# Performance work log

Hardware: AMD Instinct MI355X
Metric: run time of the kernel (lower is better)

The kernel has to match this reference:

```python
import jax, jax.numpy as jnp
import numpy as np

B, L, D = 16, 2048, 64

def setup_inputs() -> dict:
    key = jax.random.key(0)
    kq, kk, kv = jax.random.split(key, 3)
    q = jax.random.normal(kq, (B, L, D), dtype=jnp.float32)
    k = jax.random.normal(kk, (B, L, D), dtype=jnp.float32)
    v = jax.random.normal(kv, (B, L, D), dtype=jnp.float32)
    return {"q": q, "k": k, "v": v}

def reference(q, k, v):
    # scores: [B, L_q, L_k] = q @ k^T  (no scale applied, faithful to source)
    scores = jnp.einsum("bqd,bkd->bqk", q, k)
    attention = jax.nn.softmax(scores, axis=2)
    # dropout p=0.0 -> identity
    # source returns (v, attention), NOT the context
    return (v, attention)
```

## Files before the change

kernel.cpp:

```cpp
#include <hip/hip_runtime.h>
#include <hip/hip_bf16.h>

typedef short s16x8 __attribute__((ext_vector_type(8)));
typedef float f32x4 __attribute__((ext_vector_type(4)));

#define B_ 16
#define L_ 2048
#define D_ 64
#define V_ELEMS (B_ * L_ * D_)

__device__ __forceinline__ unsigned rne1(float f) {
    unsigned u = __builtin_bit_cast(unsigned, f);
    return (u + 0x7FFFu + ((u >> 16) & 1u)) >> 16;
}
__device__ __forceinline__ unsigned pack2(float a, float b) {
    return (rne1(a) & 0xFFFFu) | (rne1(b) << 16);
}

__device__ __forceinline__ void split8(float4 a, float4 b, s16x8& hi, s16x8& lo) {
    float f[8] = {a.x, a.y, a.z, a.w, b.x, b.y, b.z, b.w};
    s16x8 h, l;
#pragma unroll
    for (int i = 0; i < 8; ++i) {
        unsigned u = __builtin_bit_cast(unsigned, f[i]);
        h[i] = (short)(u >> 16);
        float lf = f[i] - __builtin_bit_cast(float, u & 0xFFFF0000u);
        l[i] = (short)rne1(lf);
    }
    hi = h; lo = l;
}

__global__ void copy_v_kernel(const float4* __restrict__ v, float4* __restrict__ o) {
    int i = blockIdx.x * blockDim.x + threadIdx.x;
    o[i] = v[i];
}

__global__ void prep_qk_kernel(const float4* __restrict__ q, const float4* __restrict__ k,
                               uint2* __restrict__ qhi, uint2* __restrict__ qlo,
                               uint2* __restrict__ khi, uint2* __restrict__ klo) {
    int i = blockIdx.x * blockDim.x + threadIdx.x;
    float4 fq = q[i];
    float4 fk = k[i];
    unsigned u0 = __builtin_bit_cast(unsigned, fq.x), u1 = __builtin_bit_cast(unsigned, fq.y);
    unsigned u2 = __builtin_bit_cast(unsigned, fq.z), u3 = __builtin_bit_cast(unsigned, fq.w);
    qhi[i] = make_uint2((u0 >> 16) | (u1 & 0xFFFF0000u), (u2 >> 16) | (u3 & 0xFFFF0000u));
    qlo[i] = make_uint2(
        pack2(fq.x - __builtin_bit_cast(float, u0 & 0xFFFF0000u),
              fq.y - __builtin_bit_cast(float, u1 & 0xFFFF0000u)),
        pack2(fq.z - __builtin_bit_cast(float, u2 & 0xFFFF0000u),
              fq.w - __builtin_bit_cast(float, u3 & 0xFFFF0000u)));
    u0 = __builtin_bit_cast(unsigned, fk.x); u1 = __builtin_bit_cast(unsigned, fk.y);
    u2 = __builtin_bit_cast(unsigned, fk.z); u3 = __builtin_bit_cast(unsigned, fk.w);
    khi[i] = make_uint2((u0 >> 16) | (u1 & 0xFFFF0000u), (u2 >> 16) | (u3 & 0xFFFF0000u));
    klo[i] = make_uint2(
        pack2(fk.x - __builtin_bit_cast(float, u0 & 0xFFFF0000u),
              fk.y - __builtin_bit_cast(float, u1 & 0xFFFF0000u)),
        pack2(fk.z - __builtin_bit_cast(float, u2 & 0xFFFF0000u),
              fk.w - __builtin_bit_cast(float, u3 & 0xFFFF0000u)));
}

__device__ __forceinline__ void store4f(float* p, unsigned u0, unsigned u1, float inv) {
    float4 w;
    w.x = __builtin_bit_cast(float, u0 << 16) * inv;
    w.y = __builtin_bit_cast(float, u0 & 0xFFFF0000u) * inv;
    w.z = __builtin_bit_cast(float, u1 << 16) * inv;
    w.w = __builtin_bit_cast(float, u1 & 0xFFFF0000u) * inv;
    *(float4*)p = w;
}

template <bool PRE>
__global__ __launch_bounds__(256, 2) void attn_kernel(
    const float* __restrict__ qf, const float* __restrict__ kf,
    const ushort* __restrict__ qhi, const ushort* __restrict__ qlo,
    const ushort* __restrict__ khi, const ushort* __restrict__ klo,
    float* __restrict__ og) {
    const int b    = blockIdx.x >> 6;
    const int q0   = (blockIdx.x & 63) << 5;
    const int tid  = threadIdx.x;
    const int wave = tid >> 6;
    const int lane = tid & 63;
    const int nq   = lane & 15;
    const int quad = lane >> 4;

    s16x8 bhi[2][2], blo[2][2];
#pragma unroll
    for (int t = 0; t < 2; ++t) {
        const size_t off = ((size_t)(b * L_ + q0 + t * 16 + nq)) * D_ + quad * 8;
        if constexpr (PRE) {
            bhi[t][0] = *(const s16x8*)(qhi + off);
            bhi[t][1] = *(const s16x8*)(qhi + off + 32);
            blo[t][0] = *(const s16x8*)(qlo + off);
            blo[t][1] = *(const s16x8*)(qlo + off + 32);
        } else {
            float4 a0 = *(const float4*)(qf + off), a1 = *(const float4*)(qf + off + 4);
            float4 a2 = *(const float4*)(qf + off + 32), a3 = *(const float4*)(qf + off + 36);
            split8(a0, a1, bhi[t][0], blo[t][0]);
            split8(a2, a3, bhi[t][1], blo[t][1]);
        }
    }

    const size_t krow0 = (size_t)b * L_ + (size_t)wave * 512 + nq;
    float s0 = 0.0f, s1 = 0.0f;
    unsigned pk0[64], pk1[64];

#pragma unroll
    for (int t = 0; t < 32; ++t) {
        const size_t off = (krow0 + (size_t)t * 16) * D_ + quad * 8;
        s16x8 ahi0, ahi1, alo0, alo1;
        if constexpr (PRE) {
            ahi0 = *(const s16x8*)(khi + off);
            ahi1 = *(const s16x8*)(khi + off + 32);
            alo0 = *(const s16x8*)(klo + off);
            alo1 = *(const s16x8*)(klo + off + 32);
        } else {
            float4 a0 = *(const float4*)(kf + off), a1 = *(const float4*)(kf + off + 4);
            float4 a2 = *(const float4*)(kf + off + 32), a3 = *(const float4*)(kf + off + 36);
            split8(a0, a1, ahi0, alo0);
            split8(a2, a3, ahi1, alo1);
        }
        f32x4 c0 = {0.f, 0.f, 0.f, 0.f}, c1 = {0.f, 0.f, 0.f, 0.f};
        c0 = __builtin_amdgcn_mfma_f32_16x16x32_bf16(ahi0, bhi[0][0], c0, 0, 0, 0);
        c0 = __builtin_amdgcn_mfma_f32_16x16x32_bf16(ahi1, bhi[0][1], c0, 0, 0, 0);
        c0 = __builtin_amdgcn_mfma_f32_16x16x32_bf16(ahi0, blo[0][0], c0, 0, 0, 0);
        c0 = __builtin_amdgcn_mfma_f32_16x16x32_bf16(ahi1, blo[0][1], c0, 0, 0, 0);
        c0 = __builtin_amdgcn_mfma_f32_16x16x32_bf16(alo0, bhi[0][0], c0, 0, 0, 0);
        c0 = __builtin_amdgcn_mfma_f32_16x16x32_bf16(alo1, bhi[0][1], c0, 0, 0, 0);
        c1 = __builtin_amdgcn_mfma_f32_16x16x32_bf16(ahi0, bhi[1][0], c1, 0, 0, 0);
        c1 = __builtin_amdgcn_mfma_f32_16x16x32_bf16(ahi1, bhi[1][1], c1, 0, 0, 0);
        c1 = __builtin_amdgcn_mfma_f32_16x16x32_bf16(ahi0, blo[1][0], c1, 0, 0, 0);
        c1 = __builtin_amdgcn_mfma_f32_16x16x32_bf16(ahi1, blo[1][1], c1, 0, 0, 0);
        c1 = __builtin_amdgcn_mfma_f32_16x16x32_bf16(alo0, bhi[1][0], c1, 0, 0, 0);
        c1 = __builtin_amdgcn_mfma_f32_16x16x32_bf16(alo1, bhi[1][1], c1, 0, 0, 0);
        float e0 = __expf(c0[0]), e1 = __expf(c0[1]), e2 = __expf(c0[2]), e3 = __expf(c0[3]);
        s0 += (e0 + e1) + (e2 + e3);
        pk0[2 * t]     = pack2(e0, e1);
        pk0[2 * t + 1] = pack2(e2, e3);
        float g0 = __expf(c1[0]), g1 = __expf(c1[1]), g2 = __expf(c1[2]), g3 = __expf(c1[3]);
        s1 += (g0 + g1) + (g2 + g3);
        pk1[2 * t]     = pack2(g0, g1);
        pk1[2 * t + 1] = pack2(g2, g3);
    }

    s0 += __shfl_xor(s0, 16); s0 += __shfl_xor(s0, 32);
    s1 += __shfl_xor(s1, 16); s1 += __shfl_xor(s1, 32);
    __shared__ float wsum[4][2][16];
    if (lane < 16) { wsum[wave][0][lane] = s0; wsum[wave][1][lane] = s1; }
    __syncthreads();
    const float inv0 = 1.0f / ((wsum[0][0][nq] + wsum[1][0][nq]) + (wsum[2][0][nq] + wsum[3][0][nq]));
    const float inv1 = 1.0f / ((wsum[0][1][nq] + wsum[1][1][nq]) + (wsum[2][1][nq] + wsum[3][1][nq]));

    float* op0 = og + ((size_t)(b * L_ + q0 + nq)) * L_ + wave * 512 + quad * 4;
    float* op1 = op0 + (size_t)16 * L_;
#pragma unroll
    for (int t = 0; t < 32; ++t) {
        store4f(op0, pk0[2 * t], pk0[2 * t + 1], inv0); op0 += 16;
        store4f(op1, pk1[2 * t], pk1[2 * t + 1], inv1); op1 += 16;
    }
}

extern "C" void kernel_launch(void* const* d_in, const int* in_sizes, int n_in,
                              void* d_out, int out_size, void* d_ws, size_t ws_size,
                              hipStream_t stream) {
    const float* q = (const float*)d_in[0];
    const float* k = (const float*)d_in[1];
    const float* v = (const float*)d_in[2];
    float* out = (float*)d_out;

    copy_v_kernel<<<dim3(V_ELEMS / 4 / 256), dim3(256), 0, stream>>>(
        (const float4*)v, (float4*)out);

    float* att = out + (size_t)V_ELEMS;
    const size_t plane = (size_t)V_ELEMS;
    const size_t need  = 4 * plane * sizeof(ushort);
    ushort* qhi = (ushort*)d_ws;
    ushort* qlo = qhi + plane;
    ushort* khi = qlo + plane;
    ushort* klo = khi + plane;

    if (ws_size >= need) {
        prep_qk_kernel<<<dim3(V_ELEMS / 4 / 256), dim3(256), 0, stream>>>(
            (const float4*)q, (const float4*)k,
            (uint2*)qhi, (uint2*)qlo, (uint2*)khi, (uint2*)klo);
        attn_kernel<true><<<dim3(B_ * (L_ / 32)), dim3(256), 0, stream>>>(
            q, k, qhi, qlo, khi, klo, att);
    } else {
        attn_kernel<false><<<dim3(B_ * (L_ / 32)), dim3(256), 0, stream>>>(
            q, k, qhi, qlo, khi, klo, att);
    }
}
```

Before: 381.8 us.

## Recompute scores in second pass instead of holding packed exps in registers

Removes the 128-register per-thread buffer of bf16-packed exponentials and instead recomputes the QK^T MFMAs and exps in a second pass to write normalized outputs. Raises launch bounds to 4 blocks per SM and partially unrolls loops to cut register pressure and raise occupancy. This doubles MFMA and K-load work but also drops the bf16 rounding of the stored probabilities, which improves accuracy.

Result: slower. 401.0 us (+5.0%).

```diff
diff --git a/kernel.cpp b/kernel.cpp
--- a/kernel.cpp
+++ b/kernel.cpp
@@ -59,17 +59,8 @@
               fk.w - __builtin_bit_cast(float, u3 & 0xFFFF0000u)));
 }
 
-__device__ __forceinline__ void store4f(float* p, unsigned u0, unsigned u1, float inv) {
-    float4 w;
-    w.x = __builtin_bit_cast(float, u0 << 16) * inv;
-    w.y = __builtin_bit_cast(float, u0 & 0xFFFF0000u) * inv;
-    w.z = __builtin_bit_cast(float, u1 << 16) * inv;
-    w.w = __builtin_bit_cast(float, u1 & 0xFFFF0000u) * inv;
-    *(float4*)p = w;
-}
-
 template <bool PRE>
-__global__ __launch_bounds__(256, 2) void attn_kernel(
+__global__ __launch_bounds__(256, 4) void attn_kernel(
     const float* __restrict__ qf, const float* __restrict__ kf,
     const ushort* __restrict__ qhi, const ushort* __restrict__ qlo,
     const ushort* __restrict__ khi, const ushort* __restrict__ klo,
@@ -100,10 +91,9 @@
     }
 
     const size_t krow0 = (size_t)b * L_ + (size_t)wave * 512 + nq;
+
     float s0 = 0.0f, s1 = 0.0f;
-    unsigned pk0[64], pk1[64];
-
-#pragma unroll
+#pragma unroll 4
     for (int t = 0; t < 32; ++t) {
         const size_t off = (krow0 + (size_t)t * 16) * D_ + quad * 8;
         s16x8 ahi0, ahi1, alo0, alo1;
@@ -131,14 +121,8 @@
         c1 = __builtin_amdgcn_mfma_f32_16x16x32_bf16(ahi1, blo[1][1], c1, 0, 0, 0);
         c1 = __builtin_amdgcn_mfma_f32_16x16x32_bf16(alo0, bhi[1][0], c1, 0, 0, 0);
         c1 = __builtin_amdgcn_mfma_f32_16x16x32_bf16(alo1, bhi[1][1], c1, 0, 0, 0);
-        float e0 = __expf(c0[0]), e1 = __expf(c0[1]), e2 = __expf(c0[2]), e3 = __expf(c0[3]);
-        s0 += (e0 + e1) + (e2 + e3);
-        pk0[2 * t]     = pack2(e0, e1);
-        pk0[2 * t + 1] = pack2(e2, e3);
-        float g0 = __expf(c1[0]), g1 = __expf(c1[1]), g2 = __expf(c1[2]), g3 = __expf(c1[3]);
-        s1 += (g0 + g1) + (g2 + g3);
-        pk1[2 * t]     = pack2(g0, g1);
-        pk1[2 * t + 1] = pack2(g2, g3);
+        s0 += (__expf(c0[0]) + __expf(c0[1])) + (__expf(c0[2]) + __expf(c0[3]));
+        s1 += (__expf(c1[0]) + __expf(c1[1])) + (__expf(c1[2]) + __expf(c1[3]));
     }
 
     s0 += __shfl_xor(s0, 16); s0 += __shfl_xor(s0, 32);
@@ -151,10 +135,41 @@
 
     float* op0 = og + ((size_t)(b * L_ + q0 + nq)) * L_ + wave * 512 + quad * 4;
     float* op1 = op0 + (size_t)16 * L_;
-#pragma unroll
+#pragma unroll 4
     for (int t = 0; t < 32; ++t) {
-        store4f(op0, pk0[2 * t], pk0[2 * t + 1], inv0); op0 += 16;
-        store4f(op1, pk1[2 * t], pk1[2 * t + 1], inv1); op1 += 16;
+        const size_t off = (krow0 + (size_t)t * 16) * D_ + quad * 8;
+        s16x8 ahi0, ahi1, alo0, alo1;
+        if constexpr (PRE) {
+            ahi0 = *(const s16x8*)(khi + off);
+            ahi1 = *(const s16x8*)(khi + off + 32);
+            alo0 = *(const s16x8*)(klo + off);
+            alo1 = *(const s16x8*)(klo + off + 32);
+        } else {
+            float4 a0 = *(const float4*)(kf + off), a1 = *(const float4*)(kf + off + 4);
+            float4 a2 = *(const float4*)(kf + off + 32), a3 = *(const float4*)(kf + off + 36);
+            split8(a0, a1, ahi0, alo0);
+            split8(a2, a3, ahi1, alo1);
+        }
+        f32x4 c0 = {0.f, 0.f, 0.f, 0.f}, c1 = {0.f, 0.f, 0.f, 0.f};
+        c0 = __builtin_amdgcn_mfma_f32_16x16x32_bf16(ahi0, bhi[0][0], c0, 0, 0, 0);
+        c0 = __builtin_amdgcn_mfma_f32_16x16x32_bf16(ahi1, bhi[0][1], c0, 0, 0, 0);
+        c0 = __builtin_amdgcn_mfma_f32_16x16x32_bf16(ahi0, blo[0][0], c0, 0, 0, 0);
+        c0 = __builtin_amdgcn_mfma_f32_16x16x32_bf16(ahi1, blo[0][1], c0, 0, 0, 0);
+        c0 = __builtin_amdgcn_mfma_f32_16x16x32_bf16(alo0, bhi[0][0], c0, 0, 0, 0);
+        c0 = __builtin_amdgcn_mfma_f32_16x16x32_bf16(alo1, bhi[0][1], c0, 0, 0, 0);
+        c1 = __builtin_amdgcn_mfma_f32_16x16x32_bf16(ahi0, bhi[1][0], c1, 0, 0, 0);
+        c1 = __builtin_amdgcn_mfma_f32_16x16x32_bf16(ahi1, bhi[1][1], c1, 0, 0, 0);
+        c1 = __builtin_amdgcn_mfma_f32_16x16x32_bf16(ahi0, blo[1][0], c1, 0, 0, 0);
+        c1 = __builtin_amdgcn_mfma_f32_16x16x32_bf16(ahi1, blo[1][1], c1, 0, 0, 0);
+        c1 = __builtin_amdgcn_mfma_f32_16x16x32_bf16(alo0, bhi[1][0], c1, 0, 0, 0);
+        c1 = __builtin_amdgcn_mfma_f32_16x16x32_bf16(alo1, bhi[1][1], c1, 0, 0, 0);
+        float4 w0, w1;
+        w0.x = __expf(c0[0]) * inv0; w0.y = __expf(c0[1]) * inv0;
+        w0.z = __expf(c0[2]) * inv0; w0.w = __expf(c0[3]) * inv0;
+        w1.x = __expf(c1[0]) * inv1; w1.y = __expf(c1[1]) * inv1;
+        w1.z = __expf(c1[2]) * inv1; w1.w = __expf(c1[3]) * inv1;
+        *(float4*)op0 = w0; op0 += 16;
+        *(float4*)op1 = w1; op1 += 16;
     }
 }
 
```
